# Kernel optimization log

Measured on AMD Instinct MI355X. Metric: run time of the kernel, lower is better.

## Reference

```python
import jax, jax.numpy as jnp
import numpy as np

B, S, H = 8, 2048, 1024
D = H // 16  # head_size = hidden_size // n_heads = 64


def setup_inputs() -> dict:
    key = jax.random.key(0)
    ks = jax.random.split(key, 7)
    scale = 1.0 / np.sqrt(H)
    x = jax.random.normal(ks[0], (B, S, H), dtype=jnp.float32)
    mask = jnp.ones((B, S), dtype=jnp.int32)
    Wq = jax.random.uniform(ks[1], (H, D), jnp.float32, -scale, scale)
    bq = jax.random.uniform(ks[2], (D,), jnp.float32, -scale, scale)
    Wk = jax.random.uniform(ks[3], (H, D), jnp.float32, -scale, scale)
    bk = jax.random.uniform(ks[4], (D,), jnp.float32, -scale, scale)
    Wv = jax.random.uniform(ks[5], (H, D), jnp.float32, -scale, scale)
    bv = jax.random.uniform(ks[6], (D,), jnp.float32, -scale, scale)
    return {"x": x, "mask": mask, "Wq": Wq, "bq": bq, "Wk": Wk, "bk": bk, "Wv": Wv, "bv": bv}


def reference(x, mask, Wq, bq, Wk, bk, Wv, bv):
    # projections: [B,S,H] @ [H,D] -> [B,S,D]
    q = jnp.einsum("bsh,hd->bsd", x, Wq) + bq
    k = jnp.einsum("bsh,hd->bsd", x, Wk) + bk
    v = jnp.einsum("bsh,hd->bsd", x, Wv) + bv
    # scores: [B,S,S]
    scores = jnp.einsum("bqd,bkd->bqk", q, k) / jnp.sqrt(jnp.asarray(q.shape[-1], q.dtype))
    # mask: [B,S] -> [B,1,S]; fill masked keys with -inf
    scores = jnp.where(mask[:, None, :] == 0, -jnp.inf, scores)
    attn = jax.nn.softmax(scores, axis=-1)
    # dropout prob is 0.0 (inference semantics) -> identity
    return jnp.einsum("bqk,bkd->bqd", attn, v)
```

## Files before the change

### kernel.cpp

```cpp
#include <hip/hip_runtime.h>

typedef __bf16 bf16x8 __attribute__((ext_vector_type(8)));
typedef __bf16 bf16x4 __attribute__((ext_vector_type(4)));
typedef float f32x4 __attribute__((ext_vector_type(4)));
typedef float f32x16 __attribute__((ext_vector_type(16)));
typedef unsigned short u16x8 __attribute__((ext_vector_type(8)));

#define MFMA16(a, b, c) __builtin_amdgcn_mfma_f32_16x16x32_bf16((a), (b), (c), 0, 0, 0)
#define MFMA32(a, b, c) __builtin_amdgcn_mfma_f32_32x32x16_bf16((a), (b), (c), 0, 0, 0)

static __device__ __forceinline__ unsigned short f2bf(float f) {
  unsigned int u = __float_as_uint(f);
  u += 0x7fffu + ((u >> 16) & 1u);
  return (unsigned short)(u >> 16);
}
static __device__ __forceinline__ float bf2f(unsigned short s) {
  return __uint_as_float((unsigned int)s << 16);
}
static __device__ __forceinline__ unsigned int cvtpk(float lo, float hi) {
  unsigned int r;
  asm("v_cvt_pk_bf16_f32 %0, %1, %2" : "=v"(r) : "v"(lo), "v"(hi));
  return r;
}
static __device__ __forceinline__ void plswap(unsigned int& a, unsigned int& b) {
  asm("v_permlane32_swap_b32 %0, %1" : "+v"(a), "+v"(b));
}

static __device__ __forceinline__ void gld_lds16(const void* g, void* l) {
  __builtin_amdgcn_global_load_lds(
      (const __attribute__((address_space(1))) unsigned int*)(g),
      (__attribute__((address_space(3))) unsigned int*)(l), 16, 0, 0);
}

__global__ __launch_bounds__(128) void wt_kernel(
    const float* __restrict__ Wq, const float* __restrict__ Wk,
    const float* __restrict__ Wv, unsigned short* __restrict__ Wt,
    const int* __restrict__ mask, float* __restrict__ mAddG) {
  const int bid = blockIdx.x;
  if (bid >= 192) {
    const int idx = (bid - 192) * 128 + threadIdx.x;
    mAddG[idx] = mask[idx] ? 0.0f : -__builtin_inff();
    return;
  }
  const int n = bid;
  const int jl = threadIdx.x;
  const float* W;
  int col;
  float scale;
  if (n < 64)       { W = Wq; col = n;       scale = 0.125f; }
  else if (n < 128) { W = Wk; col = n - 64;  scale = 1.0f; }
  else              { W = Wv; col = n - 128; scale = 1.0f; }
  const int js = (jl & ~7) | ((jl & 7) ^ (n & 7));
  u16x8 o;
#pragma unroll
  for (int e = 0; e < 8; ++e) o[e] = f2bf(W[(jl * 8 + e) * 64 + col] * scale);
  *reinterpret_cast<u16x8*>(&Wt[n * 1024 + js * 8]) = o;
}

__global__ __launch_bounds__(512, 4) void qkv_kernel(
    const float* __restrict__ x, const unsigned short* __restrict__ Wt,
    const float* __restrict__ bq, const float* __restrict__ bk,
    const float* __restrict__ bv, unsigned short* __restrict__ Q,
    unsigned short* __restrict__ K, unsigned short* __restrict__ Vt) {
  __shared__ __align__(16) unsigned short xs[2][32][72];
  __shared__ __align__(16) unsigned short ws[2][192 * 64];
  const int tid = threadIdx.x;
  const int w = tid >> 6, lane = tid & 63;
  const int lr = lane & 15, lg = lane >> 4;
  const int wg = w >> 2, wc = w & 3;
  const int m0 = blockIdx.x * 32;

  const int xrow = tid >> 4, xc4 = (tid & 15) * 4;
  const float* xsrc = x + (m0 + xrow) * 1024 + xc4;
  const unsigned short* wsrc0 = Wt + ((0 * 512 + tid) >> 3) * 1024 + (tid & 7) * 8;
  const unsigned short* wsrc1 = Wt + ((1 * 512 + tid) >> 3) * 1024 + (tid & 7) * 8;
  const unsigned short* wsrc2 = Wt + ((2 * 512 + tid) >> 3) * 1024 + (tid & 7) * 8;

  f32x4 acc[3] = {};
  const int arow = wg * 16 + lr;

#define WSTAGE(k0, buf)                                                      \
  do {                                                                       \
    gld_lds16(wsrc0 + (k0), (char*)(&ws[buf][0]) + w * 1024);                \
    gld_lds16(wsrc1 + (k0), (char*)(&ws[buf][0]) + 8192 + w * 1024);         \
    gld_lds16(wsrc2 + (k0), (char*)(&ws[buf][0]) + 16384 + w * 1024);        \
  } while (0)
#define XWRITE(v, buf)                                                       \
  do {                                                                       \
    bf16x4 xb;                                                               \
    xb[0] = (__bf16)(v).x; xb[1] = (__bf16)(v).y;                            \
    xb[2] = (__bf16)(v).z; xb[3] = (__bf16)(v).w;                            \
    *reinterpret_cast<bf16x4*>(&xs[buf][xrow][xc4]) = xb;                    \
  } while (0)

  float4 xrA = *reinterpret_cast<const float4*>(xsrc);
  WSTAGE(0, 0);
  XWRITE(xrA, 0);
  xrA = *reinterpret_cast<const float4*>(xsrc + 64);
  asm volatile("s_waitcnt vmcnt(1) lgkmcnt(0)" ::: "memory");
  __builtin_amdgcn_s_barrier();

#pragma unroll
  for (int t = 0; t < 16; ++t) {
    const int cur = t & 1;
    if (t < 15) WSTAGE((t + 1) * 64, cur ^ 1);
    __builtin_amdgcn_sched_barrier(0);
    float4 xrB = {};
    if (t < 14)
      xrB = *reinterpret_cast<const float4*>(xsrc + (t + 2) * 64);
    __builtin_amdgcn_sched_barrier(0);

    bf16x8 a[2];
#pragma unroll
    for (int kh = 0; kh < 2; ++kh)
      a[kh] = *reinterpret_cast<const bf16x8*>(&xs[cur][arow][kh * 32 + lg * 8]);
#pragma unroll
    for (int cf = 0; cf < 3; ++cf) {
      const int n = wc * 48 + cf * 16 + lr;
      const unsigned short* wr = &ws[cur][n * 64];
#pragma unroll
      for (int kh = 0; kh < 2; ++kh) {
        const int sc = (kh * 4 + lg) ^ (n & 7);
        bf16x8 bv8 = *reinterpret_cast<const bf16x8*>(wr + sc * 8);
        acc[cf] = MFMA16(a[kh], bv8, acc[cf]);
      }
    }
    if (t < 15) {
      XWRITE(xrA, cur ^ 1);
      if (t < 14)
        asm volatile("s_waitcnt vmcnt(1) lgkmcnt(0)" ::: "memory");
      else
        asm volatile("s_waitcnt vmcnt(0) lgkmcnt(0)" ::: "memory");
      __builtin_amdgcn_s_barrier();
      xrA = xrB;
    }
  }
#undef WSTAGE
#undef XWRITE

  const int mb = m0 + wg * 16 + lg * 4;
  const int b = m0 >> 11;
#pragma unroll
  for (int cf = 0; cf < 3; ++cf) {
    const int n = wc * 48 + cf * 16 + lr;
    if (n < 64) {
      const float bias = bq[n] * 0.125f;
#pragma unroll
      for (int i = 0; i < 4; ++i) Q[(mb + i) * 64 + n] = f2bf(acc[cf][i] + bias);
    } else if (n < 128) {
      const int nn = n - 64;
      const float bias = bk[nn];
#pragma unroll
      for (int i = 0; i < 4; ++i) K[(mb + i) * 64 + nn] = f2bf(acc[cf][i] + bias);
    } else {
      const int d = n - 128;
      const float bias = bv[d];
      ushort4 o;
      o.x = f2bf(acc[cf][0] + bias);
      o.y = f2bf(acc[cf][1] + bias);
      o.z = f2bf(acc[cf][2] + bias);
      o.w = f2bf(acc[cf][3] + bias);
      const int sl = (m0 & 2047) + wg * 16 + lg * 4;
      *reinterpret_cast<ushort4*>(&Vt[((b * 64 + d) << 11) + sl]) = o;
    }
  }
}

__global__ __launch_bounds__(256) void attn_kernel(
    const unsigned short* __restrict__ Q, const unsigned short* __restrict__ K,
    const unsigned short* __restrict__ Vt, const float* __restrict__ mAddG,
    unsigned short* __restrict__ Opb, float* __restrict__ mp,
    float* __restrict__ lp) {
  __shared__ __align__(16) unsigned short ks[64][72];
  __shared__ __align__(16) unsigned short vs[64][72];

  const int qt = blockIdx.x, b = blockIdx.y, c = blockIdx.z;
  const int tid = threadIdx.x;
  const int w = tid >> 6, lane = tid & 63;
  const int l31 = lane & 31, h = lane >> 5;
  const int bh = b * 2048;
  const int qb = qt * 128 + w * 32;
  const int sr = tid >> 3, scc = (tid & 7) * 8;

  bf16x8 qf[4];
#pragma unroll
  for (int dt = 0; dt < 4; ++dt)
    qf[dt] = *reinterpret_cast<const bf16x8*>(
        &Q[(bh + qb + l31) * 64 + dt * 16 + h * 8]);

  uint4 rk0, rk1, rv0, rv1;
  {
    const int kv0 = c * 512;
    rk0 = *reinterpret_cast<const uint4*>(&K[(bh + kv0 + sr) * 64 + scc]);
    rk1 = *reinterpret_cast<const uint4*>(&K[(bh + kv0 + 32 + sr) * 64 + scc]);
    rv0 = *reinterpret_cast<const uint4*>(&Vt[(b * 64 + sr) * 2048 + kv0 + scc]);
    rv1 = *reinterpret_cast<const uint4*>(&Vt[(b * 64 + 32 + sr) * 2048 + kv0 + scc]);
  }

  f32x16 oacc[2] = {};
  float m_s = -__builtin_inff(), l_s = 0.0f;

  for (int it = 0; it < 8; ++it) {
    const int kv0 = c * 512 + it * 64;
    __builtin_amdgcn_s_barrier();

    f32x4 md0[4], md1[4];
#pragma unroll
    for (int rb = 0; rb < 4; ++rb) {
      md0[rb] = *reinterpret_cast<const f32x4*>(&mAddG[bh + kv0 + rb * 8 + 4 * h]);
      md1[rb] = *reinterpret_cast<const f32x4*>(&mAddG[bh + kv0 + 32 + rb * 8 + 4 * h]);
    }

    *reinterpret_cast<uint4*>(&ks[sr][scc]) = rk0;
    *reinterpret_cast<uint4*>(&ks[32 + sr][scc]) = rk1;
    *reinterpret_cast<uint4*>(&vs[sr][scc]) = rv0;
    *reinterpret_cast<uint4*>(&vs[32 + sr][scc]) = rv1;

    if (it < 7) {
      const int kvn = kv0 + 64;
      rk0 = *reinterpret_cast<const uint4*>(&K[(bh + kvn + sr) * 64 + scc]);
      rk1 = *reinterpret_cast<const uint4*>(&K[(bh + kvn + 32 + sr) * 64 + scc]);
      rv0 = *reinterpret_cast<const uint4*>(&Vt[(b * 64 + sr) * 2048 + kvn + scc]);
      rv1 = *reinterpret_cast<const uint4*>(&Vt[(b * 64 + 32 + sr) * 2048 + kvn + scc]);
    }

    asm volatile("s_waitcnt lgkmcnt(0)" ::: "memory");
    __builtin_amdgcn_s_barrier();

    f32x16 st0 = {}, st1 = {};
    __builtin_amdgcn_s_setprio(1);
#pragma unroll
    for (int dt = 0; dt < 4; ++dt) {
      const bf16x8 kf0 = *reinterpret_cast<const bf16x8*>(&ks[l31][dt * 16 + h * 8]);
      st0 = MFMA32(kf0, qf[dt], st0);
    }
#pragma unroll
    for (int dt = 0; dt < 4; ++dt) {
      const bf16x8 kf1 = *reinterpret_cast<const bf16x8*>(&ks[32 + l31][dt * 16 + h * 8]);
      st1 = MFMA32(kf1, qf[dt], st1);
    }
    __builtin_amdgcn_s_setprio(0);

#pragma unroll
    for (int rb = 0; rb < 4; ++rb)
#pragma unroll
      for (int j = 0; j < 4; ++j) {
        st0[rb * 4 + j] += md0[rb][j];
        st1[rb * 4 + j] += md1[rb][j];
      }

    float pm = st0[0];
#pragma unroll
    for (int r = 1; r < 16; ++r) pm = fmaxf(pm, st0[r]);
#pragma unroll
    for (int r = 0; r < 16; ++r) pm = fmaxf(pm, st1[r]);
    pm = fmaxf(pm, __shfl_xor(pm, 32));
    const float nm = fmaxf(m_s, pm);
    if (!__all(nm <= m_s + 8.0f)) {
      const float scn = __expf(m_s - nm);
      m_s = nm;
      l_s *= scn;
#pragma unroll
      for (int r = 0; r < 16; ++r) {
        const float scr = __shfl(scn, (r & 3) + 8 * (r >> 2) + 4 * h);
        oacc[0][r] *= scr;
        oacc[1][r] *= scr;
      }
    }
    const float mexp = (m_s == -__builtin_inff()) ? 0.0f : m_s;
    float rs = 0.0f;
#pragma unroll
    for (int r = 0; r < 16; ++r) {
      const float p0 = __expf(st0[r] - mexp);
      st0[r] = p0;
      rs += p0;
      const float p1 = __expf(st1[r] - mexp);
      st1[r] = p1;
      rs += p1;
    }
    rs += __shfl_xor(rs, 32);
    l_s += rs;

    unsigned int paw[4][4];
#pragma unroll
    for (int kt16 = 0; kt16 < 4; ++kt16) {
      const int lo = kt16 & 1;
      unsigned int X0, X1, Y0, Y1;
      if (kt16 < 2) {
        X0 = cvtpk(st0[lo * 8 + 0], st0[lo * 8 + 1]);
        Y0 = cvtpk(st0[lo * 8 + 2], st0[lo * 8 + 3]);
        X1 = cvtpk(st0[lo * 8 + 4], st0[lo * 8 + 5]);
        Y1 = cvtpk(st0[lo * 8 + 6], st0[lo * 8 + 7]);
      } else {
        X0 = cvtpk(st1[lo * 8 + 0], st1[lo * 8 + 1]);
        Y0 = cvtpk(st1[lo * 8 + 2], st1[lo * 8 + 3]);
        X1 = cvtpk(st1[lo * 8 + 4], st1[lo * 8 + 5]);
        Y1 = cvtpk(st1[lo * 8 + 6], st1[lo * 8 + 7]);
      }
      plswap(X0, X1);
      plswap(Y0, Y1);
      paw[kt16][0] = X0;
      paw[kt16][1] = Y0;
      paw[kt16][2] = X1;
      paw[kt16][3] = Y1;
    }

    __builtin_amdgcn_s_setprio(1);
#pragma unroll
    for (int nf = 0; nf < 2; ++nf)
#pragma unroll
      for (int kt16 = 0; kt16 < 4; ++kt16) {
        const bf16x8 vb = *reinterpret_cast<const bf16x8*>(
            &vs[nf * 32 + l31][kt16 * 16 + h * 8]);
        const bf16x8 pa = *reinterpret_cast<const bf16x8*>(&paw[kt16][0]);
        oacc[nf] = MFMA32(pa, vb, oacc[nf]);
      }
    __builtin_amdgcn_s_setprio(0);
  }

  const float inv_s = (l_s > 0.0f) ? 1.0f / l_s : 0.0f;
#pragma unroll
  for (int r = 0; r < 16; ++r) {
    const int qoff = (r & 3) + 8 * (r >> 2) + 4 * h;
    const float invr = __shfl(inv_s, qoff);
    const int row = bh + qb + qoff;
    Opb[(c * 16384 + row) * 64 + l31] = f2bf(oacc[0][r] * invr);
    Opb[(c * 16384 + row) * 64 + 32 + l31] = f2bf(oacc[1][r] * invr);
  }
  if (h == 0) {
    mp[c * 16384 + bh + qb + l31] = m_s;
    lp[c * 16384 + bh + qb + l31] = l_s;
  }
}

__global__ __launch_bounds__(256) void merge_kernel(
    const unsigned short* __restrict__ Opb, const float* __restrict__ mp,
    const float* __restrict__ lp, float* __restrict__ out) {
  const int t = blockIdx.x * 256 + threadIdx.x;
  const int row = t >> 4;
  const int cc = (t & 15) * 4;
  float mv[4], lv[4];
#pragma unroll
  for (int c = 0; c < 4; ++c) {
    mv[c] = mp[c * 16384 + row];
    lv[c] = lp[c * 16384 + row];
  }
  float M = fmaxf(fmaxf(mv[0], mv[1]), fmaxf(mv[2], mv[3]));
  float L = 0.0f;
  f32x4 o = {};
#pragma unroll
  for (int c = 0; c < 4; ++c) {
    const float wc = __expf(mv[c] - M) * lv[c];
    L += wc;
    const ushort4 u = *reinterpret_cast<const ushort4*>(
        &Opb[(c * 16384 + row) * 64 + cc]);
    f32x4 oc;
    oc[0] = bf2f(u.x); oc[1] = bf2f(u.y); oc[2] = bf2f(u.z); oc[3] = bf2f(u.w);
    o += oc * wc;
  }
  const float inv = 1.0f / L;
  *reinterpret_cast<f32x4*>(&out[row * 64 + cc]) = o * inv;
}

extern "C" void kernel_launch(void* const* d_in, const int* in_sizes, int n_in,
                              void* d_out, int out_size, void* d_ws, size_t ws_size,
                              hipStream_t stream) {
  const float* x  = (const float*)d_in[0];
  const int* mask = (const int*)d_in[1];
  const float* Wq = (const float*)d_in[2];
  const float* bq = (const float*)d_in[3];
  const float* Wk = (const float*)d_in[4];
  const float* bk = (const float*)d_in[5];
  const float* Wv = (const float*)d_in[6];
  const float* bv = (const float*)d_in[7];
  float* out = (float*)d_out;

  unsigned short* Wt = (unsigned short*)d_ws;
  unsigned short* Qw = Wt + 192 * 1024;
  unsigned short* Kw = Qw + 16384 * 64;
  unsigned short* Vt = Kw + 16384 * 64;
  unsigned short* Opb = Vt + 16384 * 64;
  float* mAddG = (float*)(Opb + 4 * 16384 * 64);
  float* mp = mAddG + 16384;
  float* lp = mp + 4 * 16384;

  hipLaunchKernelGGL(wt_kernel, dim3(320), dim3(128), 0, stream,
                     Wq, Wk, Wv, Wt, mask, mAddG);
  hipLaunchKernelGGL(qkv_kernel, dim3(512), dim3(512), 0, stream,
                     x, Wt, bq, bk, bv, Qw, Kw, Vt);
  hipLaunchKernelGGL(attn_kernel, dim3(16, 8, 4), dim3(256), 0, stream,
                     Qw, Kw, Vt, mAddG, Opb, mp, lp);
  hipLaunchKernelGGL(merge_kernel, dim3(1024), dim3(256), 0, stream,
                     Opb, mp, lp, out);
}
```

Measured before the change: 49.33 us.

## Split QKV by column halves, double KV splits, use exp2 and skip unmasked tiles

The QKV projection is split into two blocks per row tile, each covering half of the 192 output columns. This doubles the grid and lowers per-block LDS. Attention splits keys into 8 chunks instead of 4 to double parallelism, with the merge widened to 8 partials. A per-block ballot skips the additive mask load when the chunk has no masked keys. Softmax now uses exp2 with log2e folded into the Q scale, and a raised rescale-deferral threshold. The cost is more partial-output traffic, more merge work, and x being read twice by the QKV kernel.

New measurement: 57.83 us. 1.17x slower.

```diff
diff --git a/kernel.cpp b/kernel.cpp
--- a/kernel.cpp
+++ b/kernel.cpp
@@ -8,6 +8,13 @@
 
 #define MFMA16(a, b, c) __builtin_amdgcn_mfma_f32_16x16x32_bf16((a), (b), (c), 0, 0, 0)
 #define MFMA32(a, b, c) __builtin_amdgcn_mfma_f32_32x32x16_bf16((a), (b), (c), 0, 0, 0)
+
+#define SCALE_Q 0.180336880f
+#define DEFER_TH 11.5415603f
+
+static __device__ __forceinline__ float fexp2(float x) {
+  return __builtin_amdgcn_exp2f(x);
+}
 
 static __device__ __forceinline__ unsigned short f2bf(float f) {
   unsigned int u = __float_as_uint(f);
@@ -47,7 +54,7 @@
   const float* W;
   int col;
   float scale;
-  if (n < 64)       { W = Wq; col = n;       scale = 0.125f; }
+  if (n < 64)       { W = Wq; col = n;       scale = SCALE_Q; }
   else if (n < 128) { W = Wk; col = n - 64;  scale = 1.0f; }
   else              { W = Wv; col = n - 128; scale = 1.0f; }
   const int js = (jl & ~7) | ((jl & 7) ^ (n & 7));
@@ -57,47 +64,58 @@
   *reinterpret_cast<u16x8*>(&Wt[n * 1024 + js * 8]) = o;
 }
 
-__global__ __launch_bounds__(512, 4) void qkv_kernel(
+__global__ __launch_bounds__(256, 4) void qkv_kernel(
     const float* __restrict__ x, const unsigned short* __restrict__ Wt,
     const float* __restrict__ bq, const float* __restrict__ bk,
     const float* __restrict__ bv, unsigned short* __restrict__ Q,
     unsigned short* __restrict__ K, unsigned short* __restrict__ Vt) {
   __shared__ __align__(16) unsigned short xs[2][32][72];
-  __shared__ __align__(16) unsigned short ws[2][192 * 64];
+  __shared__ __align__(16) unsigned short ws[2][96 * 64];
   const int tid = threadIdx.x;
   const int w = tid >> 6, lane = tid & 63;
   const int lr = lane & 15, lg = lane >> 4;
-  const int wg = w >> 2, wc = w & 3;
-  const int m0 = blockIdx.x * 32;
-
-  const int xrow = tid >> 4, xc4 = (tid & 15) * 4;
-  const float* xsrc = x + (m0 + xrow) * 1024 + xc4;
-  const unsigned short* wsrc0 = Wt + ((0 * 512 + tid) >> 3) * 1024 + (tid & 7) * 8;
-  const unsigned short* wsrc1 = Wt + ((1 * 512 + tid) >> 3) * 1024 + (tid & 7) * 8;
-  const unsigned short* wsrc2 = Wt + ((2 * 512 + tid) >> 3) * 1024 + (tid & 7) * 8;
+  const int wg = w >> 1, wc = w & 1;
+  const int m0 = (blockIdx.x >> 1) * 32;
+  const int nh = blockIdx.x & 1;
+
+  const int xr0 = tid >> 4, xcc0 = (tid & 15) * 4;
+  const int xr1 = (256 + tid) >> 4, xcc1 = ((256 + tid) & 15) * 4;
+  const float* xsrc0 = x + (m0 + xr0) * 1024 + xcc0;
+  const float* xsrc1 = x + (m0 + xr1) * 1024 + xcc1;
+  const unsigned short* wsrc0 =
+      Wt + (nh * 96 + ((0 * 256 + tid) >> 3)) * 1024 + (tid & 7) * 8;
+  const unsigned short* wsrc1 =
+      Wt + (nh * 96 + ((1 * 256 + tid) >> 3)) * 1024 + (tid & 7) * 8;
+  const unsigned short* wsrc2 =
+      Wt + (nh * 96 + ((2 * 256 + tid) >> 3)) * 1024 + (tid & 7) * 8;
 
   f32x4 acc[3] = {};
   const int arow = wg * 16 + lr;
 
-#define WSTAGE(k0, buf)                                                      \
-  do {                                                                       \
-    gld_lds16(wsrc0 + (k0), (char*)(&ws[buf][0]) + w * 1024);                \
-    gld_lds16(wsrc1 + (k0), (char*)(&ws[buf][0]) + 8192 + w * 1024);         \
-    gld_lds16(wsrc2 + (k0), (char*)(&ws[buf][0]) + 16384 + w * 1024);        \
+#define WSTAGE(k0, buf)                                                       \
+  do {                                                                        \
+    gld_lds16(wsrc0 + (k0), (char*)(&ws[buf][0]) + (0 * 256 + w * 64) * 16);  \
+    gld_lds16(wsrc1 + (k0), (char*)(&ws[buf][0]) + (1 * 256 + w * 64) * 16);  \
+    gld_lds16(wsrc2 + (k0), (char*)(&ws[buf][0]) + (2 * 256 + w * 64) * 16);  \
   } while (0)
-#define XWRITE(v, buf)                                                       \
-  do {                                                                       \
-    bf16x4 xb;                                                               \
-    xb[0] = (__bf16)(v).x; xb[1] = (__bf16)(v).y;                            \
-    xb[2] = (__bf16)(v).z; xb[3] = (__bf16)(v).w;                            \
-    *reinterpret_cast<bf16x4*>(&xs[buf][xrow][xc4]) = xb;                    \
+#define XWRITE(v0, v1, buf)                                                   \
+  do {                                                                        \
+    bf16x4 t0, t1;                                                            \
+    t0[0] = (__bf16)(v0).x; t0[1] = (__bf16)(v0).y;                           \
+    t0[2] = (__bf16)(v0).z; t0[3] = (__bf16)(v0).w;                           \
+    t1[0] = (__bf16)(v1).x; t1[1] = (__bf16)(v1).y;                           \
+    t1[2] = (__bf16)(v1).z; t1[3] = (__bf16)(v1).w;                           \
+    *reinterpret_cast<bf16x4*>(&xs[buf][xr0][xcc0]) = t0;                     \
+    *reinterpret_cast<bf16x4*>(&xs[buf][xr1][xcc1]) = t1;                     \
   } while (0)
 
-  float4 xrA = *reinterpret_cast<const float4*>(xsrc);
+  float4 xrA0 = *reinterpret_cast<const float4*>(xsrc0);
+  float4 xrA1 = *reinterpret_cast<const float4*>(xsrc1);
   WSTAGE(0, 0);
-  XWRITE(xrA, 0);
-  xrA = *reinterpret_cast<const float4*>(xsrc + 64);
-  asm volatile("s_waitcnt vmcnt(1) lgkmcnt(0)" ::: "memory");
+  XWRITE(xrA0, xrA1, 0);
+  xrA0 = *reinterpret_cast<const float4*>(xsrc0 + 64);
+  xrA1 = *reinterpret_cast<const float4*>(xsrc1 + 64);
+  asm volatile("s_waitcnt vmcnt(2) lgkmcnt(0)" ::: "memory");
   __builtin_amdgcn_s_barrier();
 
 #pragma unroll
@@ -105,9 +123,11 @@
     const int cur = t & 1;
     if (t < 15) WSTAGE((t + 1) * 64, cur ^ 1);
     __builtin_amdgcn_sched_barrier(0);
-    float4 xrB = {};
-    if (t < 14)
-      xrB = *reinterpret_cast<const float4*>(xsrc + (t + 2) * 64);
+    float4 xrB0 = {}, xrB1 = {};
+    if (t < 14) {
+      xrB0 = *reinterpret_cast<const float4*>(xsrc0 + (t + 2) * 64);
+      xrB1 = *reinterpret_cast<const float4*>(xsrc1 + (t + 2) * 64);
+    }
     __builtin_amdgcn_sched_barrier(0);
 
     bf16x8 a[2];
@@ -116,23 +136,24 @@
       a[kh] = *reinterpret_cast<const bf16x8*>(&xs[cur][arow][kh * 32 + lg * 8]);
 #pragma unroll
     for (int cf = 0; cf < 3; ++cf) {
-      const int n = wc * 48 + cf * 16 + lr;
-      const unsigned short* wr = &ws[cur][n * 64];
+      const int nl = wc * 48 + cf * 16 + lr;
+      const unsigned short* wr = &ws[cur][nl * 64];
 #pragma unroll
       for (int kh = 0; kh < 2; ++kh) {
-        const int sc = (kh * 4 + lg) ^ (n & 7);
+        const int sc = (kh * 4 + lg) ^ (nl & 7);
         bf16x8 bv8 = *reinterpret_cast<const bf16x8*>(wr + sc * 8);
         acc[cf] = MFMA16(a[kh], bv8, acc[cf]);
       }
     }
     if (t < 15) {
-      XWRITE(xrA, cur ^ 1);
+      XWRITE(xrA0, xrA1, cur ^ 1);
       if (t < 14)
-        asm volatile("s_waitcnt vmcnt(1) lgkmcnt(0)" ::: "memory");
+        asm volatile("s_waitcnt vmcnt(2) lgkmcnt(0)" ::: "memory");
       else
         asm volatile("s_waitcnt vmcnt(0) lgkmcnt(0)" ::: "memory");
       __builtin_amdgcn_s_barrier();
-      xrA = xrB;
+      xrA0 = xrB0;
+      xrA1 = xrB1;
     }
   }
 #undef WSTAGE
@@ -142,9 +163,9 @@
   const int b = m0 >> 11;
 #pragma unroll
   for (int cf = 0; cf < 3; ++cf) {
-    const int n = wc * 48 + cf * 16 + lr;
+    const int n = nh * 96 + wc * 48 + cf * 16 + lr;
     if (n < 64) {
-      const float bias = bq[n] * 0.125f;
+      const float bias = bq[n] * SCALE_Q;
 #pragma unroll
       for (int i = 0; i < 4; ++i) Q[(mb + i) * 64 + n] = f2bf(acc[cf][i] + bias);
     } else if (n < 128) {
@@ -166,13 +187,14 @@
   }
 }
 
-__global__ __launch_bounds__(256) void attn_kernel(
+__global__ __launch_bounds__(256, 3) void attn_kernel(
     const unsigned short* __restrict__ Q, const unsigned short* __restrict__ K,
     const unsigned short* __restrict__ Vt, const float* __restrict__ mAddG,
-    unsigned short* __restrict__ Opb, float* __restrict__ mp,
-    float* __restrict__ lp) {
+    const int* __restrict__ maskI, unsigned short* __restrict__ Opb,
+    float* __restrict__ mp, float* __restrict__ lp) {
   __shared__ __align__(16) unsigned short ks[64][72];
   __shared__ __align__(16) unsigned short vs[64][72];
+  __shared__ int fl[4];
 
   const int qt = blockIdx.x, b = blockIdx.y, c = blockIdx.z;
   const int tid = threadIdx.x;
@@ -182,6 +204,14 @@
   const int qb = qt * 128 + w * 32;
   const int sr = tid >> 3, scc = (tid & 7) * 8;
 
+  {
+    const int mz = (maskI[bh + c * 256 + tid] == 0) ? 1 : 0;
+    const unsigned long long bal = __ballot(mz);
+    if (lane == 0) fl[w] = (bal != 0ull) ? 1 : 0;
+  }
+  __syncthreads();
+  const bool hasMask = (fl[0] | fl[1] | fl[2] | fl[3]) != 0;
+
   bf16x8 qf[4];
 #pragma unroll
   for (int dt = 0; dt < 4; ++dt)
@@ -190,7 +220,7 @@
 
   uint4 rk0, rk1, rv0, rv1;
   {
-    const int kv0 = c * 512;
+    const int kv0 = c * 256;
     rk0 = *reinterpret_cast<const uint4*>(&K[(bh + kv0 + sr) * 64 + scc]);
     rk1 = *reinterpret_cast<const uint4*>(&K[(bh + kv0 + 32 + sr) * 64 + scc]);
     rv0 = *reinterpret_cast<const uint4*>(&Vt[(b * 64 + sr) * 2048 + kv0 + scc]);
@@ -200,23 +230,16 @@
   f32x16 oacc[2] = {};
   float m_s = -__builtin_inff(), l_s = 0.0f;
 
-  for (int it = 0; it < 8; ++it) {
-    const int kv0 = c * 512 + it * 64;
+  for (int it = 0; it < 4; ++it) {
+    const int kv0 = c * 256 + it * 64;
     __builtin_amdgcn_s_barrier();
-
-    f32x4 md0[4], md1[4];
-#pragma unroll
-    for (int rb = 0; rb < 4; ++rb) {
-      md0[rb] = *reinterpret_cast<const f32x4*>(&mAddG[bh + kv0 + rb * 8 + 4 * h]);
-      md1[rb] = *reinterpret_cast<const f32x4*>(&mAddG[bh + kv0 + 32 + rb * 8 + 4 * h]);
-    }
 
     *reinterpret_cast<uint4*>(&ks[sr][scc]) = rk0;
     *reinterpret_cast<uint4*>(&ks[32 + sr][scc]) = rk1;
     *reinterpret_cast<uint4*>(&vs[sr][scc]) = rv0;
     *reinterpret_cast<uint4*>(&vs[32 + sr][scc]) = rv1;
 
-    if (it < 7) {
+    if (it < 3) {
       const int kvn = kv0 + 64;
       rk0 = *reinterpret_cast<const uint4*>(&K[(bh + kvn + sr) * 64 + scc]);
       rk1 = *reinterpret_cast<const uint4*>(&K[(bh + kvn + 32 + sr) * 64 + scc]);
@@ -241,13 +264,20 @@
     }
     __builtin_amdgcn_s_setprio(0);
 
-#pragma unroll
-    for (int rb = 0; rb < 4; ++rb)
-#pragma unroll
-      for (int j = 0; j < 4; ++j) {
-        st0[rb * 4 + j] += md0[rb][j];
-        st1[rb * 4 + j] += md1[rb][j];
+    if (hasMask) {
+#pragma unroll
+      for (int rb = 0; rb < 4; ++rb) {
+        const f32x4 md0 =
+            *reinterpret_cast<const f32x4*>(&mAddG[bh + kv0 + rb * 8 + 4 * h]);
+        const f32x4 md1 = *reinterpret_cast<const f32x4*>(
+            &mAddG[bh + kv0 + 32 + rb * 8 + 4 * h]);
+#pragma unroll
+        for (int j = 0; j < 4; ++j) {
+          st0[rb * 4 + j] += md0[j];
+          st1[rb * 4 + j] += md1[j];
+        }
       }
+    }
 
     float pm = st0[0];
 #pragma unroll
@@ -256,8 +286,8 @@
     for (int r = 0; r < 16; ++r) pm = fmaxf(pm, st1[r]);
     pm = fmaxf(pm, __shfl_xor(pm, 32));
     const float nm = fmaxf(m_s, pm);
-    if (!__all(nm <= m_s + 8.0f)) {
-      const float scn = __expf(m_s - nm);
+    if (!__all(nm <= m_s + DEFER_TH)) {
+      const float scn = fexp2(m_s - nm);
       m_s = nm;
       l_s *= scn;
 #pragma unroll
@@ -271,10 +301,10 @@
     float rs = 0.0f;
 #pragma unroll
     for (int r = 0; r < 16; ++r) {
-      const float p0 = __expf(st0[r] - mexp);
+      const float p0 = fexp2(st0[r] - mexp);
       st0[r] = p0;
       rs += p0;
-      const float p1 = __expf(st1[r] - mexp);
+      const float p1 = fexp2(st1[r] - mexp);
       st1[r] = p1;
       rs += p1;
     }
@@ -339,18 +369,20 @@
   const int t = blockIdx.x * 256 + threadIdx.x;
   const int row = t >> 4;
   const int cc = (t & 15) * 4;
-  float mv[4], lv[4];
-#pragma unroll
-  for (int c = 0; c < 4; ++c) {
+  float mv[8], lv[8];
+#pragma unroll
+  for (int c = 0; c < 8; ++c) {
     mv[c] = mp[c * 16384 + row];
     lv[c] = lp[c * 16384 + row];
   }
-  float M = fmaxf(fmaxf(mv[0], mv[1]), fmaxf(mv[2], mv[3]));
+  float M = mv[0];
+#pragma unroll
+  for (int c = 1; c < 8; ++c) M = fmaxf(M, mv[c]);
   float L = 0.0f;
   f32x4 o = {};
 #pragma unroll
-  for (int c = 0; c < 4; ++c) {
-    const float wc = __expf(mv[c] - M) * lv[c];
+  for (int c = 0; c < 8; ++c) {
+    const float wc = __builtin_amdgcn_exp2f(mv[c] - M) * lv[c];
     L += wc;
     const ushort4 u = *reinterpret_cast<const ushort4*>(
         &Opb[(c * 16384 + row) * 64 + cc]);
@@ -380,16 +412,16 @@
   unsigned short* Kw = Qw + 16384 * 64;
   unsigned short* Vt = Kw + 16384 * 64;
   unsigned short* Opb = Vt + 16384 * 64;
-  float* mAddG = (float*)(Opb + 4 * 16384 * 64);
+  float* mAddG = (float*)(Opb + 8 * 16384 * 64);
   float* mp = mAddG + 16384;
-  float* lp = mp + 4 * 16384;
+  float* lp = mp + 8 * 16384;
 
   hipLaunchKernelGGL(wt_kernel, dim3(320), dim3(128), 0, stream,
                      Wq, Wk, Wv, Wt, mask, mAddG);
-  hipLaunchKernelGGL(qkv_kernel, dim3(512), dim3(512), 0, stream,
+  hipLaunchKernelGGL(qkv_kernel, dim3(1024), dim3(256), 0, stream,
                      x, Wt, bq, bk, bv, Qw, Kw, Vt);
-  hipLaunchKernelGGL(attn_kernel, dim3(16, 8, 4), dim3(256), 0, stream,
-                     Qw, Kw, Vt, mAddG, Opb, mp, lp);
+  hipLaunchKernelGGL(attn_kernel, dim3(16, 8, 8), dim3(256), 0, stream,
+                     Qw, Kw, Vt, mAddG, mask, Opb, mp, lp);
   hipLaunchKernelGGL(merge_kernel, dim3(1024), dim3(256), 0, stream,
                      Opb, mp, lp, out);
 }
```
